# Performance work log

Hardware: AMD Instinct MI355X
Metric: run time of the kernel (lower is better)

The kernel has to match this reference:

```python
import jax, jax.numpy as jnp
import numpy as np

B, S, D, H = 4, 2048, 1024, 16
DK = D // H
THETA = 10000.0

def _trunc_normal(key, shape, in_f, out_f):
    std = (2.0 / (in_f + out_f)) ** 0.5
    return jax.random.truncated_normal(key, -3.0, 3.0, shape, jnp.float32) * std

def setup_inputs() -> dict:
    key = jax.random.key(0)
    kx, kq, kk, kv, ko = jax.random.split(key, 5)
    x = jax.random.normal(kx, (B, S, D), jnp.float32)
    wq = _trunc_normal(kq, (D, D), D, D)
    wk = _trunc_normal(kk, (D, D), D, D)
    wv = _trunc_normal(kv, (D, D), D, D)
    wo = _trunc_normal(ko, (D, D), D, D)
    token_positions = jnp.arange(S, dtype=jnp.int32)
    return {"x": x, "wq": wq, "wk": wk, "wv": wv, "wo": wo,
            "token_positions": token_positions}

def _rope_tables(token_positions, d_k, theta):
    # freq_cos/sin with each frequency duplicated pairwise: (d j) layout
    exponent = jnp.arange(0, d_k, 2, dtype=jnp.float32) / d_k
    freq = 1.0 / (theta ** exponent)            # [d_k/2]
    f = token_positions.astype(jnp.float32)[:, None] * freq[None, :]  # [s, d_k/2]
    cos = jnp.repeat(jnp.cos(f), 2, axis=-1)    # [s, d_k]
    sin = jnp.repeat(jnp.sin(f), 2, axis=-1)
    return cos, sin

def _rotate_half(x):
    x_even = x[..., 0::2]
    x_odd = x[..., 1::2]
    return jnp.stack((-x_odd, x_even), axis=-1).reshape(x.shape)

def reference(x, wq, wk, wv, wo, token_positions):
    b, s, d = x.shape
    # projections: y = x @ W^T  (weight stored [out, in])
    def proj(w):
        y = jnp.einsum('bsi,oi->bso', x, w)
        return y.reshape(b, s, H, DK).transpose(0, 2, 1, 3)  # [b,h,s,dk]
    q, k, v = proj(wq), proj(wk), proj(wv)
    cos, sin = _rope_tables(token_positions, DK, THETA)      # [s,dk]
    q = q * cos + _rotate_half(q) * sin
    k = k * cos + _rotate_half(k) * sin
    scores = jnp.einsum('bhnd,bhmd->bhnm', q, k) / jnp.sqrt(jnp.float32(DK))
    mask = jnp.tril(jnp.ones((s, s), dtype=bool))
    scores = jnp.where(mask, scores, -jnp.inf)
    attn = jax.nn.softmax(scores, axis=-1)
    out = jnp.einsum('bhnm,bhmd->bhnd', attn, v)
    out = out.transpose(0, 2, 1, 3).reshape(b, s, d)
    return jnp.einsum('bsi,oi->bso', out, wo)
```

## Files before the change

kernel.cpp:

```cpp
#include <hip/hip_runtime.h>
#include <hip/hip_bf16.h>
#include <stdint.h>
#include <math.h>

static constexpr int kS  = 2048;
static constexpr int kH  = 16;
static constexpr int kDK = 64;
static constexpr int kD  = 1024;
static constexpr int kB  = 4;
static constexpr int kM  = kB * kS;

typedef __bf16 bf16;
typedef __attribute__((ext_vector_type(8))) __bf16 bf16x8;
typedef __attribute__((ext_vector_type(4))) __bf16 bf16x4;
typedef __attribute__((ext_vector_type(4))) float f32x4;

__device__ __forceinline__ void gload_lds16(const bf16* g, bf16* l) {
  __builtin_amdgcn_global_load_lds((__attribute__((address_space(1))) void*)(void*)g,
                                   (__attribute__((address_space(3))) void*)l, 16, 0, 0);
}

__global__ void cvt_f32_bf16(const float* __restrict__ in, bf16* __restrict__ out, int n4) {
  int i = blockIdx.x * blockDim.x + threadIdx.x;
  if (i >= n4) return;
  float4 v = reinterpret_cast<const float4*>(in)[i];
  bf16x4 o;
  o[0] = (bf16)v.x; o[1] = (bf16)v.y; o[2] = (bf16)v.z; o[3] = (bf16)v.w;
  reinterpret_cast<bf16x4*>(out)[i] = o;
}

__global__ void cvt_w4(const float* __restrict__ w0, const float* __restrict__ w1,
                       const float* __restrict__ w2, const float* __restrict__ w3,
                       bf16* __restrict__ o0, bf16* __restrict__ o1,
                       bf16* __restrict__ o2, bf16* __restrict__ o3, int n4) {
  int i = blockIdx.x * blockDim.x + threadIdx.x;
  if (i >= n4) return;
  const int sel = blockIdx.y;
  const float* in = (sel == 0) ? w0 : (sel == 1) ? w1 : (sel == 2) ? w2 : w3;
  bf16* out      = (sel == 0) ? o0 : (sel == 1) ? o1 : (sel == 2) ? o2 : o3;
  float4 v = reinterpret_cast<const float4*>(in)[i];
  bf16x4 o;
  o[0] = (bf16)v.x; o[1] = (bf16)v.y; o[2] = (bf16)v.z; o[3] = (bf16)v.w;
  reinterpret_cast<bf16x4*>(out)[i] = o;
}

template<int BM>
__device__ __forceinline__ void gemm_body(const bf16* __restrict__ A,
                                          const bf16* __restrict__ W,
                                          void* __restrict__ dst,
                                          int K, int mode, int brow, int bcol) {
  constexpr int MF  = BM / 32;
  constexpr int ACH = BM / 64;

  __shared__ __align__(16) bf16 As[3][BM * 32];
  __shared__ __align__(16) bf16 Bs[3][128 * 32];

  const int tid = threadIdx.x;
  const int l   = tid & 63;
  const int w   = tid >> 6;
  const int wr = (w >> 1) * (BM / 2);
  const int wc = (w & 1) * 64;

  f32x4 acc[MF][4] = {};

  const int lrow = l >> 2;
  const int lcol = (l & 3) * 8;
  const int fr  = l & 15;
  const int fk  = (l >> 4) * 8;

  const int nk = K >> 5;

  auto STAGE = [&](int buf, int kt) {
    const int k0 = kt << 5;
#pragma unroll
    for (int c2 = 0; c2 < ACH; ++c2) {
      const int c = w * ACH + c2;
      gload_lds16(A + (size_t)(brow + c * 16 + lrow) * K + k0 + lcol, &As[buf][c * 512]);
    }
#pragma unroll
    for (int c2 = 0; c2 < 2; ++c2) {
      const int c = w * 2 + c2;
      gload_lds16(W + (size_t)(bcol + c * 16 + lrow) * K + k0 + lcol, &Bs[buf][c * 512]);
    }
  };

  STAGE(0, 0);
  STAGE(1, 1);

  int cur = 0;
  for (int kt = 0; kt < nk; ++kt) {
    if (kt + 1 < nk) { asm volatile("s_waitcnt vmcnt(4)" ::: "memory"); }
    else             { asm volatile("s_waitcnt vmcnt(0)" ::: "memory"); }
    __builtin_amdgcn_s_barrier();
    __builtin_amdgcn_sched_barrier(0);

    if (kt + 2 < nk) {
      int s2 = cur + 2; if (s2 >= 3) s2 -= 3;
      STAGE(s2, kt + 2);
    }

    bf16x8 af[MF], bfm[4];
#pragma unroll
    for (int m = 0; m < MF; ++m) af[m]  = *(const bf16x8*)&As[cur][(wr + m * 16 + fr) * 32 + fk];
#pragma unroll
    for (int n = 0; n < 4; ++n)  bfm[n] = *(const bf16x8*)&Bs[cur][(wc + n * 16 + fr) * 32 + fk];
#pragma unroll
    for (int m = 0; m < MF; ++m)
#pragma unroll
      for (int n = 0; n < 4; ++n)
        acc[m][n] = __builtin_amdgcn_mfma_f32_16x16x32_bf16(af[m], bfm[n], acc[m][n], 0, 0, 0);

    cur = (cur + 1 == 3) ? 0 : cur + 1;
  }

  const int frow = (l >> 4) * 4;
  if (mode == 0) {
    bf16* out = (bf16*)dst;
#pragma unroll
    for (int m = 0; m < MF; ++m) {
#pragma unroll
      for (int n = 0; n < 4; ++n) {
        const int col = bcol + wc + n * 16 + fr;
        const int h = col >> 6, dk = col & 63;
#pragma unroll
        for (int r = 0; r < 4; ++r) {
          const int row = brow + wr + m * 16 + frow + r;
          const int b = row >> 11, s = row & (kS - 1);
          out[((((size_t)b * kH + h) * kS + s) << 6) + dk] = (bf16)acc[m][n][r];
        }
      }
    }
  } else {
    float* out = (float*)dst;
#pragma unroll
    for (int m = 0; m < MF; ++m) {
#pragma unroll
      for (int n = 0; n < 4; ++n) {
        const int col = bcol + wc + n * 16 + fr;
#pragma unroll
        for (int r = 0; r < 4; ++r) {
          const int row = brow + wr + m * 16 + frow + r;
          out[(size_t)row * kD + col] = acc[m][n][r];
        }
      }
    }
  }
}

template<int BM>
__global__ __launch_bounds__(256) void gemm_k(const bf16* __restrict__ A,
                                              const bf16* __restrict__ W,
                                              void* __restrict__ dst, int K, int mode) {
  gemm_body<BM>(A, W, dst, K, mode, blockIdx.x * BM, blockIdx.y * 128);
}

__global__ __launch_bounds__(256) void gemm_qkv(const bf16* __restrict__ A,
                                                const bf16* __restrict__ wq,
                                                const bf16* __restrict__ wk,
                                                const bf16* __restrict__ wv,
                                                bf16* __restrict__ Qb,
                                                bf16* __restrict__ Kb,
                                                bf16* __restrict__ Vb, int K) {
  const int by = blockIdx.y;
  const int sel = by >> 3;
  const bf16* W = (sel == 0) ? wq : (sel == 1) ? wk : wv;
  bf16* dst     = (sel == 0) ? Qb : (sel == 1) ? Kb : Vb;
  gemm_body<128>(A, W, dst, K, 0, blockIdx.x * 128, (by & 7) * 128);
}

__global__ void rope_kernel(bf16* __restrict__ Q, bf16* __restrict__ Kb,
                            const int* __restrict__ pos, int np) {
  int idx = blockIdx.x * blockDim.x + threadIdx.x;
  if (idx >= 2 * np) return;
  const bool isQ = (idx < np);
  bf16* T = isQ ? Q : Kb;
  int id = isQ ? idx : idx - np;
  const int i = id & 31;
  const int s = (id >> 5) & (kS - 1);
  const float p = (float)pos[s];
  const float freq = __expf(-0.2878231366242557f * (float)i);
  const float frev = p * freq * 0.15915494309189535f;
  const float r = frev - floorf(frev);
  const float sn = __builtin_amdgcn_sinf(r);
  const float cs = __builtin_amdgcn_cosf(r);
  const float sc = isQ ? (0.125f * 1.4426950408889634f) : 1.0f;
  const size_t off = (size_t)id * 2;
  const float e = (float)T[off], o = (float)T[off + 1];
  T[off]     = (bf16)((e * cs - o * sn) * sc);
  T[off + 1] = (bf16)((o * cs + e * sn) * sc);
}

__global__ __launch_bounds__(256) void attn_fwd(const bf16* __restrict__ Q,
                                                const bf16* __restrict__ Kb,
                                                const bf16* __restrict__ Vb,
                                                bf16* __restrict__ O) {
  const int bh = blockIdx.x;
  const int qt = (int)gridDim.y - 1 - (int)blockIdx.y;
  const int tid = threadIdx.x;
  const int l = tid & 63;
  const int w = tid >> 6;

  __shared__ __align__(16) bf16 Ks[64 * 64];
  __shared__ __align__(16) bf16 Vt[64 * 64];
  __shared__ __align__(16) bf16 Pl[4][16 * 64];

  const int q0 = qt * 64 + w * 16;
  const int fr  = l & 15;
  const int fkg = l >> 4;
  const int fkg4 = fkg << 2;
  const size_t base = (size_t)bh * kS * kDK;

  bf16x8 aq[2];
#pragma unroll
  for (int kc = 0; kc < 2; ++kc)
    aq[kc] = *(const bf16x8*)&Q[base + (size_t)(q0 + fr) * kDK + kc * 32 + fkg * 8];

  f32x4 ao[4] = {};
  float m_r = -1e30f, l_r = 0.f;

  const int nt = qt + 1;

  const int krow = tid >> 3;
  const int kcol = (tid & 7) * 8;
  const int dk0  = w * 16;

  bf16x8 kreg0, kreg1, vreg0, vreg1;
  {
    const size_t kb0 = base + (size_t)krow * kDK + kcol;
    kreg0 = *(const bf16x8*)&Kb[kb0];
    kreg1 = *(const bf16x8*)&Kb[kb0 + 32 * kDK];
    const size_t vb0 = base + (size_t)l * kDK + dk0;
    vreg0 = *(const bf16x8*)&Vb[vb0];
    vreg1 = *(const bf16x8*)&Vb[vb0 + 8];
  }

  for (int j = 0; j < nt; ++j) {
    {
      const int r0 = krow, r1 = krow + 32;
      *(bf16x8*)&Ks[r0 * 64 + (kcol ^ ((r0 & 7) << 3))] = kreg0;
      *(bf16x8*)&Ks[r1 * 64 + (kcol ^ ((r1 & 7) << 3))] = kreg1;
#pragma unroll
      for (int e = 0; e < 8; ++e) {
        const int d0 = dk0 + e, d1 = dk0 + 8 + e;
        Vt[d0 * 64 + (l ^ ((d0 & 7) << 3))] = vreg0[e];
        Vt[d1 * 64 + (l ^ ((d1 & 7) << 3))] = vreg1[e];
      }
    }
    __syncthreads();

    if (j + 1 < nt) {
      const size_t kb0 = base + (size_t)((j + 1) * 64 + krow) * kDK + kcol;
      kreg0 = *(const bf16x8*)&Kb[kb0];
      kreg1 = *(const bf16x8*)&Kb[kb0 + 32 * kDK];
      const size_t vb0 = base + (size_t)((j + 1) * 64 + l) * kDK + dk0;
      vreg0 = *(const bf16x8*)&Vb[vb0];
      vreg1 = *(const bf16x8*)&Vb[vb0 + 8];
    }

    const bool diag = (j == nt - 1);

    f32x4 sc[4] = {};
#pragma unroll
    for (int nf = 0; nf < 4; ++nf) {
      if (!diag || nf <= w) {
#pragma unroll
        for (int kc = 0; kc < 2; ++kc) {
          const int row = nf * 16 + fr;
          bf16x8 bk = *(const bf16x8*)&Ks[row * 64 + ((kc * 32 + fkg * 8) ^ ((row & 7) << 3))];
          sc[nf] = __builtin_amdgcn_mfma_f32_16x16x32_bf16(bk, aq[kc], sc[nf], 0, 0, 0);
        }
      }
    }

    const int qloc = w * 16 + fr;
    float p[4][4];
    float mx = -INFINITY;
#pragma unroll
    for (int nf = 0; nf < 4; ++nf)
#pragma unroll
      for (int r = 0; r < 4; ++r) {
        float s = sc[nf][r];
        if (diag && (nf * 16 + fkg4 + r) > qloc) s = -INFINITY;
        p[nf][r] = s;
        mx = fmaxf(mx, s);
      }
    mx = fmaxf(mx, __shfl_xor(mx, 16));
    mx = fmaxf(mx, __shfl_xor(mx, 32));

    if (__any(mx > m_r + 11.5f)) {
      const float mnew = fmaxf(m_r, mx);
      const float sf = __builtin_amdgcn_exp2f(m_r - mnew);
      l_r *= sf;
      m_r = mnew;
#pragma unroll
      for (int r = 0; r < 4; ++r) {
        const float sfq = __shfl(sf, (l & 48) + fkg4 + r);
#pragma unroll
        for (int n = 0; n < 4; ++n) ao[n][r] *= sfq;
      }
    }

    float rs = 0.f;
#pragma unroll
    for (int nf = 0; nf < 4; ++nf)
#pragma unroll
      for (int r = 0; r < 4; ++r) {
        p[nf][r] = __builtin_amdgcn_exp2f(p[nf][r] - m_r);
        rs += p[nf][r];
      }
    rs += __shfl_xor(rs, 16);
    rs += __shfl_xor(rs, 32);
    l_r += rs;

#pragma unroll
    for (int nf = 0; nf < 4; ++nf) {
      bf16x4 p4;
#pragma unroll
      for (int r = 0; r < 4; ++r) p4[r] = (bf16)p[nf][r];
      *(bf16x4*)&Pl[w][fr * 64 + ((nf * 16 + fkg4) ^ ((fr & 7) << 3))] = p4;
    }
    bf16x8 pa[2];
#pragma unroll
    for (int kc2 = 0; kc2 < 2; ++kc2)
      pa[kc2] = *(const bf16x8*)&Pl[w][fr * 64 + ((kc2 * 32 + fkg * 8) ^ ((fr & 7) << 3))];

#pragma unroll
    for (int kc2 = 0; kc2 < 2; ++kc2) {
      if (kc2 == 0 || !diag || w >= 2) {
#pragma unroll
        for (int n = 0; n < 4; ++n) {
          const int row = n * 16 + fr;
          bf16x8 bv = *(const bf16x8*)&Vt[row * 64 + ((kc2 * 32 + fkg * 8) ^ ((row & 7) << 3))];
          ao[n] = __builtin_amdgcn_mfma_f32_16x16x32_bf16(pa[kc2], bv, ao[n], 0, 0, 0);
        }
      }
    }
    __syncthreads();
  }

  const int b = bh >> 4, h = bh & 15;
  float lq[4];
#pragma unroll
  for (int r = 0; r < 4; ++r) lq[r] = __shfl(l_r, (l & 48) + fkg4 + r);
#pragma unroll
  for (int n = 0; n < 4; ++n)
#pragma unroll
    for (int r = 0; r < 4; ++r) {
      const int qg = q0 + fkg4 + r;
      const float ov = ao[n][r] / lq[r];
      O[((size_t)(b * kS + qg) << 10) + h * 64 + n * 16 + fr] = (bf16)ov;
    }
}

extern "C" void kernel_launch(void* const* d_in, const int* in_sizes, int n_in,
                              void* d_out, int out_size, void* d_ws, size_t ws_size,
                              hipStream_t stream) {
  const float* x  = (const float*)d_in[0];
  const float* wq = (const float*)d_in[1];
  const float* wk = (const float*)d_in[2];
  const float* wv = (const float*)d_in[3];
  const float* wo = (const float*)d_in[4];
  const int* pos  = (const int*)d_in[5];

  bf16* xb  = (bf16*)d_ws;
  bf16* wqb = xb  + (size_t)kM * kD;
  bf16* wkb = wqb + (size_t)kD * kD;
  bf16* wvb = wkb + (size_t)kD * kD;
  bf16* wob = wvb + (size_t)kD * kD;
  bf16* Qb  = wob + (size_t)kD * kD;
  bf16* Kbf = Qb  + (size_t)64 * kS * kDK;
  bf16* Vbf = Kbf + (size_t)64 * kS * kDK;
  bf16* Ob  = Vbf + (size_t)64 * kS * kDK;

  {
    int n4 = kM * kD / 4;
    cvt_f32_bf16<<<(n4 + 255) / 256, 256, 0, stream>>>(x, xb, n4);
    n4 = kD * kD / 4;
    cvt_w4<<<dim3((n4 + 255) / 256, 4), 256, 0, stream>>>(wq, wk, wv, wo, wqb, wkb, wvb, wob, n4);
  }

  gemm_qkv<<<dim3(kM / 128, 24), 256, 0, stream>>>(xb, wqb, wkb, wvb, Qb, Kbf, Vbf, kD);

  const int np = 64 * kS * 32;
  rope_kernel<<<(2 * np) / 256, 256, 0, stream>>>(Qb, Kbf, pos, np);

  dim3 ga(64, kS / 64);
  attn_fwd<<<ga, 256, 0, stream>>>(Qb, Kbf, Vbf, Ob);

  gemm_k<128><<<dim3(kM / 128, kD / 128), 256, 0, stream>>>(Ob, wob, d_out, kD, 1);
}
```

Before: 278.0 us.

## Replace QKV projection GEMM with 256x256 tile, 512-thread double-buffered kernel

Swaps the shared 128x128 GEMM body used for the fused QKV projection for a dedicated kernel. The new kernel uses 256x256 output tiles, 8 waves, BK=64, double-buffered LDS filled by direct global-to-LDS loads with an XOR swizzle to avoid bank conflicts, and raises wave priority around the MFMA block. The goal is more data reuse per loaded byte and fewer barriers per FLOP in the largest GEMM. The cost is 128 KB of LDS per block and a 256-accumulator register footprint, which can limit occupancy and cause register spilling. The grid also shrinks to 384 blocks, which may leave CUs unevenly loaded.

After: 282.4 us. No clear change (+1.6%).

```diff
diff --git a/kernel.cpp b/kernel.cpp
--- a/kernel.cpp
+++ b/kernel.cpp
@@ -44,6 +44,112 @@
   reinterpret_cast<bf16x4*>(out)[i] = o;
 }
 
+__global__ __launch_bounds__(512, 2) void gemm_qkv256(const bf16* __restrict__ A,
+                                                      const bf16* __restrict__ wq,
+                                                      const bf16* __restrict__ wk,
+                                                      const bf16* __restrict__ wv,
+                                                      bf16* __restrict__ Qb,
+                                                      bf16* __restrict__ Kb,
+                                                      bf16* __restrict__ Vb, int K) {
+  __shared__ __align__(16) bf16 LA[2][256 * 64];
+  __shared__ __align__(16) bf16 LB[2][256 * 64];
+
+  const int by  = blockIdx.y;
+  const int sel = by >> 2;
+  const bf16* W = (sel == 0) ? wq : (sel == 1) ? wk : wv;
+  bf16* dst     = (sel == 0) ? Qb : (sel == 1) ? Kb : Vb;
+  const int brow = blockIdx.x * 256;
+  const int bcol = (by & 3) * 256;
+
+  const int tid = threadIdx.x;
+  const int l   = tid & 63;
+  const int w   = tid >> 6;
+  const int wm  = w >> 2;
+  const int wn  = w & 3;
+  const int fr  = l & 15;
+  const int fkg = l >> 4;
+
+  const int srow = tid >> 3;
+  const int scb  = tid & 7;
+
+  f32x4 acc[8][4] = {};
+
+  const int nk = K >> 6;
+
+  auto STAGE = [&](int buf, int kt) {
+    const int k0 = kt << 6;
+#pragma unroll
+    for (int li = 0; li < 4; ++li) {
+      const int row = li * 64 + srow;
+      const int cb  = scb ^ (row & 7);
+      gload_lds16(A + (size_t)(brow + row) * K + k0 + cb * 8,
+                  &LA[buf][li * 4096 + srow * 64 + scb * 8]);
+    }
+#pragma unroll
+    for (int li = 0; li < 4; ++li) {
+      const int row = li * 64 + srow;
+      const int cb  = scb ^ (row & 7);
+      gload_lds16(W + (size_t)(bcol + row) * K + k0 + cb * 8,
+                  &LB[buf][li * 4096 + srow * 64 + scb * 8]);
+    }
+  };
+
+  STAGE(0, 0);
+
+  int cur = 0;
+  for (int kt = 0; kt < nk; ++kt) {
+    if (kt + 1 < nk) {
+      STAGE(cur ^ 1, kt + 1);
+      asm volatile("s_waitcnt vmcnt(8)" ::: "memory");
+    } else {
+      asm volatile("s_waitcnt vmcnt(0)" ::: "memory");
+    }
+    __builtin_amdgcn_s_barrier();
+    __builtin_amdgcn_sched_barrier(0);
+
+#pragma unroll
+    for (int kc = 0; kc < 2; ++kc) {
+      bf16x8 af[8], bfr[4];
+#pragma unroll
+      for (int m = 0; m < 8; ++m) {
+        const int row = wm * 128 + m * 16 + fr;
+        af[m] = *(const bf16x8*)&LA[cur][row * 64 + (((kc * 4 + fkg) ^ (fr & 7)) * 8)];
+      }
+#pragma unroll
+      for (int n = 0; n < 4; ++n) {
+        const int row = wn * 64 + n * 16 + fr;
+        bfr[n] = *(const bf16x8*)&LB[cur][row * 64 + (((kc * 4 + fkg) ^ (fr & 7)) * 8)];
+      }
+      __builtin_amdgcn_s_setprio(1);
+#pragma unroll
+      for (int m = 0; m < 8; ++m)
+#pragma unroll
+        for (int n = 0; n < 4; ++n)
+          acc[m][n] = __builtin_amdgcn_mfma_f32_16x16x32_bf16(af[m], bfr[n], acc[m][n], 0, 0, 0);
+      __builtin_amdgcn_s_setprio(0);
+    }
+
+    __builtin_amdgcn_s_barrier();
+    cur ^= 1;
+  }
+
+  const int frow = fkg * 4;
+#pragma unroll
+  for (int m = 0; m < 8; ++m) {
+#pragma unroll
+    for (int n = 0; n < 4; ++n) {
+      const int col = bcol + wn * 64 + n * 16 + fr;
+      const int h = col >> 6, dk = col & 63;
+#pragma unroll
+      for (int r = 0; r < 4; ++r) {
+        const int row = brow + wm * 128 + m * 16 + frow + r;
+        const int b = row >> 11, s = row & (kS - 1);
+        dst[((((size_t)b * kH + h) * kS + s) << 6) + dk] = (bf16)acc[m][n][r];
+      }
+    }
+  }
+}
+
 template<int BM>
 __device__ __forceinline__ void gemm_body(const bf16* __restrict__ A,
                                           const bf16* __restrict__ W,
@@ -152,20 +258,6 @@
                                               const bf16* __restrict__ W,
                                               void* __restrict__ dst, int K, int mode) {
   gemm_body<BM>(A, W, dst, K, mode, blockIdx.x * BM, blockIdx.y * 128);
-}
-
-__global__ __launch_bounds__(256) void gemm_qkv(const bf16* __restrict__ A,
-                                                const bf16* __restrict__ wq,
-                                                const bf16* __restrict__ wk,
-                                                const bf16* __restrict__ wv,
-                                                bf16* __restrict__ Qb,
-                                                bf16* __restrict__ Kb,
-                                                bf16* __restrict__ Vb, int K) {
-  const int by = blockIdx.y;
-  const int sel = by >> 3;
-  const bf16* W = (sel == 0) ? wq : (sel == 1) ? wk : wv;
-  bf16* dst     = (sel == 0) ? Qb : (sel == 1) ? Kb : Vb;
-  gemm_body<128>(A, W, dst, K, 0, blockIdx.x * 128, (by & 7) * 128);
 }
 
 __global__ void rope_kernel(bf16* __restrict__ Q, bf16* __restrict__ Kb,
@@ -379,7 +471,7 @@
     cvt_w4<<<dim3((n4 + 255) / 256, 4), 256, 0, stream>>>(wq, wk, wv, wo, wqb, wkb, wvb, wob, n4);
   }
 
-  gemm_qkv<<<dim3(kM / 128, 24), 256, 0, stream>>>(xb, wqb, wkb, wvb, Qb, Kbf, Vbf, kD);
+  gemm_qkv256<<<dim3(kM / 256, 12), 512, 0, stream>>>(xb, wqb, wkb, wvb, Qb, Kbf, Vbf, kD);
 
   const int np = 64 * kS * 32;
   rope_kernel<<<(2 * np) / 256, 256, 0, stream>>>(Qb, Kbf, pos, np);
```
